# Kernel optimization log

Hardware: AMD Instinct MI355X
Metric: run time of the kernel (lower is better)

Reference implementation:

```python
import jax, jax.numpy as jnp
import numpy as np

NUM_HEADS = 16
MAX_BATCH = 4
MAX_SEQ = 2048


def setup_inputs() -> dict:
    key = jax.random.key(0)
    ks = jax.random.split(key, 9)
    B, S, H = 4, 2048, 2048
    scale = 0.02
    hidden_state = jax.random.normal(ks[0], (B, S, H), dtype=jnp.float32)
    # causal mask (masked_fill where mask == 0), broadcastable over batch/heads
    mask = jnp.tril(jnp.ones((S, S), dtype=jnp.int32))[None, None]  # [1,1,S,S]
    Wq = jax.random.normal(ks[1], (H, H), dtype=jnp.float32) * scale
    Wk = jax.random.normal(ks[2], (H, H), dtype=jnp.float32) * scale
    Wv = jax.random.normal(ks[3], (H, H), dtype=jnp.float32) * scale
    Wo = jax.random.normal(ks[4], (H, H), dtype=jnp.float32) * scale
    bq = jax.random.normal(ks[5], (H,), dtype=jnp.float32) * scale
    bk = jax.random.normal(ks[6], (H,), dtype=jnp.float32) * scale
    bv = jax.random.normal(ks[7], (H,), dtype=jnp.float32) * scale
    bo = jax.random.normal(ks[8], (H,), dtype=jnp.float32) * scale
    return {"hidden_state": hidden_state, "mask": mask,
            "Wq": Wq, "bq": bq, "Wk": Wk, "bk": bk,
            "Wv": Wv, "bv": bv, "Wo": Wo, "bo": bo,
            "start_pos": 0}


def reference(hidden_state, mask, Wq, bq, Wk, bk, Wv, bv, Wo, bo, start_pos):
    B, S, H = hidden_state.shape
    nh = NUM_HEADS
    hd = H // nh
    # qkv projections (nn.Linear: x @ W.T + b)
    q = (hidden_state @ Wq.T + bq).reshape(B, S, nh, hd)
    k = (hidden_state @ Wk.T + bk).reshape(B, S, nh, hd)
    v = (hidden_state @ Wv.T + bv).reshape(B, S, nh, hd)
    # KV-cache append (zeros-initialized buffer, write [start_pos:start_pos+S])
    cache_k = jnp.zeros((MAX_BATCH, MAX_SEQ, nh, hd), dtype=q.dtype)
    cache_v = jnp.zeros((MAX_BATCH, MAX_SEQ, nh, hd), dtype=q.dtype)
    cache_k = jax.lax.dynamic_update_slice(cache_k, k, (0, start_pos, 0, 0))
    cache_v = jax.lax.dynamic_update_slice(cache_v, v, (0, start_pos, 0, 0))
    total = start_pos + S
    key = cache_k[:B, :total]   # [B, total, nh, hd]
    value = cache_v[:B, :total]
    # scores: [B, nh, S, total]
    scores = jnp.einsum('bqhd,bkhd->bhqk', q, key) / jnp.sqrt(jnp.float32(hd))
    scores = jnp.where(mask == 0, -jnp.inf, scores)
    probs = jax.nn.softmax(scores, axis=-1)
    out = jnp.einsum('bhqk,bkhd->bqhd', probs, value).reshape(B, S, H)
    return out @ Wo.T + bo
```

## Files before the change

kernel.cpp:

```cpp
#include <hip/hip_runtime.h>
#include <hip/hip_bf16.h>
#include <stdint.h>

#define S_LEN 2048
#define HDIM  2048
#define NH    16
#define HD    128
#define BATCH 4

typedef __attribute__((ext_vector_type(8))) short bf16x8;
typedef __attribute__((ext_vector_type(4))) float f32x4;
typedef __attribute__((ext_vector_type(4))) float float4v;
typedef __attribute__((ext_vector_type(4))) unsigned short u16x4;

__device__ __forceinline__ void gload_lds16(const void* g, void* l) {
  __builtin_amdgcn_global_load_lds(
      (const __attribute__((address_space(1))) unsigned int*)g,
      (__attribute__((address_space(3))) unsigned int*)l,
      16, 0, 0);
}

__device__ __forceinline__ unsigned short f2bf(float x) {
  __hip_bfloat16 b = __float2bfloat16(x);
  return *reinterpret_cast<unsigned short*>(&b);
}

#define SL2E 0.1275174465f

__global__ __launch_bounds__(256) void cvt5_kernel(
    const float* __restrict__ x,
    const float* __restrict__ w0, const float* __restrict__ w1,
    const float* __restrict__ w2, const float* __restrict__ w3,
    unsigned short* __restrict__ ox,
    unsigned short* __restrict__ o0, unsigned short* __restrict__ o1,
    unsigned short* __restrict__ o2, unsigned short* __restrict__ o3,
    int n4x, int n4w) {
  const int y = blockIdx.y;
  const float* in = (y == 0) ? x : (y == 1) ? w0 : (y == 2) ? w1 : (y == 3) ? w2 : w3;
  unsigned short* out = (y == 0) ? ox : (y == 1) ? o0 : (y == 2) ? o1 : (y == 3) ? o2 : o3;
  const int n4 = (y == 0) ? n4x : n4w;
  int stride = gridDim.x * blockDim.x;
  for (int i = blockIdx.x * blockDim.x + threadIdx.x; i < n4; i += stride) {
    float4v v = *(const float4v*)(in + (size_t)i * 4);
    u16x4 o;
    o.x = f2bf(v.x); o.y = f2bf(v.y); o.z = f2bf(v.z); o.w = f2bf(v.w);
    *(u16x4*)(out + (size_t)i * 4) = o;
  }
}


#define G8_VMW(N) asm volatile("s_waitcnt vmcnt(" #N ")" ::: "memory")
#define G8_BAR1() do { __builtin_amdgcn_sched_barrier(0); __builtin_amdgcn_s_barrier(); \
  asm volatile("s_waitcnt lgkmcnt(0)" ::: "memory"); __builtin_amdgcn_sched_barrier(0); } while (0)
#define G8_BAR2() do { __builtin_amdgcn_sched_barrier(0); __builtin_amdgcn_s_barrier(); \
  __builtin_amdgcn_sched_barrier(0); } while (0)

#define G8_STAGE(ISB, BUF, HALF, KT) do {                                          \
  int kt_ = (KT); if (kt_ > nkt1) kt_ = nkt1;                                      \
  const char* gs_ = ((ISB) ? Bg : Ag) +                                            \
      (size_t)(((ISB) ? bn : bm) * 256 + (HALF) * 128 + w * 16) * (size_t)K2 +     \
      (size_t)kt_ * 128;                                                           \
  char* ld_ = lds + (BUF) * 65536 + (ISB) * 32768 + ((HALF) * 128 + w * 16) * 128; \
  gload_lds16(gs_ + sLn, ld_);                                                     \
  gload_lds16(gs_ + 8 * (size_t)K2 + sLn, ld_ + 1024);                             \
} while (0)

#define G8_RDA(BUF, MI0) do {                                                      \
  _Pragma("unroll") for (int mi = 0; mi < 4; ++mi)                                 \
  _Pragma("unroll") for (int kk = 0; kk < 2; ++kk)                                 \
    a[mi][kk] = *(const bf16x8*)(lds + (BUF) * 65536 +                             \
        (wm + ((MI0) + mi) * 16 + ln) * 128 + ((((kk << 2) + g) ^ ln7) << 4));     \
} while (0)

#define G8_RDB(BUF, NI0, BREG) do {                                                \
  _Pragma("unroll") for (int ni = 0; ni < 2; ++ni)                                 \
  _Pragma("unroll") for (int kk = 0; kk < 2; ++kk)                                 \
    BREG[ni][kk] = *(const bf16x8*)(lds + (BUF) * 65536 + 32768 +                  \
        (wn + ((NI0) + ni) * 16 + ln) * 128 + ((((kk << 2) + g) ^ ln7) << 4));     \
} while (0)

#define G8_MFMA(M0, N0, BREG) do {                                                 \
  __builtin_amdgcn_s_setprio(1);                                                   \
  _Pragma("unroll") for (int mi = 0; mi < 4; ++mi)                                 \
  _Pragma("unroll") for (int ni = 0; ni < 2; ++ni)                                 \
  _Pragma("unroll") for (int kk = 0; kk < 2; ++kk)                                 \
    acc[(M0) + mi][(N0) + ni] = __builtin_amdgcn_mfma_f32_16x16x32_bf16(           \
        a[mi][kk], BREG[ni][kk], acc[(M0) + mi][(N0) + ni], 0, 0, 0);              \
  __builtin_amdgcn_s_setprio(0);                                                   \
} while (0)

template<int OUTMODE>
__global__ __launch_bounds__(512, 2) void gemm8(
    const __hip_bfloat16* __restrict__ A, const __hip_bfloat16* __restrict__ B,
    const float* __restrict__ bias, void* __restrict__ C,
    int M, int N, int K, float scale) {
  __shared__ char lds[131072];
  const int tid = threadIdx.x;
  const int w = tid >> 6;
  const int lane = tid & 63;
  const int g = lane >> 4;
  const int ln = lane & 15;
  const int ln7 = lane & 7;
  const int K2 = K * 2;
  const int nkt = K >> 6;
  const int nkt1 = nkt - 1;
  const int niter = nkt >> 1;

  const int NBN = N >> 8;
  const int nwg = (M >> 8) * NBN;
  const int cpx = nwg >> 3;
  const int bid = blockIdx.x;
  const int wg = (bid & 7) * cpx + (bid >> 3);
  const int bm = wg / NBN, bn = wg % NBN;

  const int wm = (w >> 2) * 128;
  const int wn = (w & 3) * 64;

  const char* Ag = (const char*)A;
  const char* Bg = (const char*)B;
  const size_t sLn = (size_t)(lane >> 3) * (size_t)K2 +
                     (size_t)(((lane & 7) ^ (lane >> 3)) << 4);

  f32x4 acc[8][4];
#pragma unroll
  for (int mi = 0; mi < 8; ++mi)
#pragma unroll
    for (int ni = 0; ni < 4; ++ni) acc[mi][ni] = (f32x4){0.f, 0.f, 0.f, 0.f};

  G8_STAGE(0, 0, 0, 0); G8_STAGE(0, 0, 1, 0);
  G8_STAGE(1, 0, 0, 0); G8_STAGE(1, 0, 1, 0);
  G8_STAGE(1, 1, 0, 1); G8_STAGE(1, 1, 1, 1);
  G8_VMW(4);
  G8_BAR2();

  for (int i = 0; i < niter; ++i) {
    const int v = 2 * i + 1, u2 = 2 * i + 2, v2 = 2 * i + 3;
    bf16x8 a[4][2], b0[2][2], b1[2][2];
    G8_RDA(0, 0); G8_RDB(0, 0, b0);
    G8_STAGE(0, 1, 0, v);
    G8_BAR1();
    G8_MFMA(0, 0, b0);
    G8_BAR2();
    G8_RDB(0, 2, b1);
    G8_STAGE(0, 1, 1, v);
    G8_BAR1();
    G8_MFMA(0, 2, b1);
    G8_BAR2();
    G8_RDA(0, 4);
    G8_STAGE(1, 0, 0, u2);
    G8_BAR1();
    G8_MFMA(4, 0, b0);
    G8_BAR2();
    G8_STAGE(1, 0, 1, u2);
    G8_VMW(4);
    G8_BAR1();
    G8_MFMA(4, 2, b1);
    G8_BAR2();
    G8_RDA(1, 0); G8_RDB(1, 0, b0);
    G8_STAGE(0, 0, 0, u2);
    G8_BAR1();
    G8_MFMA(0, 0, b0);
    G8_BAR2();
    G8_RDB(1, 2, b1);
    G8_STAGE(0, 0, 1, u2);
    G8_BAR1();
    G8_MFMA(0, 2, b1);
    G8_BAR2();
    G8_RDA(1, 4);
    G8_STAGE(1, 1, 0, v2);
    G8_BAR1();
    G8_MFMA(4, 0, b0);
    G8_BAR2();
    G8_STAGE(1, 1, 1, v2);
    G8_VMW(4);
    G8_BAR1();
    G8_MFMA(4, 2, b1);
    G8_BAR2();
  }

  G8_VMW(0);
#pragma unroll
  for (int ni = 0; ni < 4; ++ni) {
    const int col = bn * 256 + wn + ni * 16 + ln;
    const float bv = bias[col];
#pragma unroll
    for (int mi = 0; mi < 8; ++mi) {
      const int row0 = bm * 256 + wm + mi * 16 + g * 4;
      if (OUTMODE == 2) {
        const int h = col >> 7, d = col & 127;
        const size_t base = ((size_t)((row0 >> 11) * NH + h) * HD + d) * S_LEN +
                            (row0 & (S_LEN - 1));
        u16x4 pk;
#pragma unroll
        for (int r = 0; r < 4; ++r)
          pk[r] = f2bf((acc[mi][ni][r] + bv) * scale);
        *(u16x4*)((unsigned short*)C + base) = pk;
      } else {
#pragma unroll
        for (int r = 0; r < 4; ++r) {
          float val = (acc[mi][ni][r] + bv) * scale;
          if (OUTMODE == 1)
            ((float*)C)[(size_t)(row0 + r) * N + col] = val;
          else
            ((__hip_bfloat16*)C)[(size_t)(row0 + r) * N + col] = __float2bfloat16(val);
        }
      }
    }
  }
}

#define DEFER_THR 8.0f

__global__ __launch_bounds__(256, 2) void attn_kernel(
    const __hip_bfloat16* __restrict__ Q, const __hip_bfloat16* __restrict__ Kg,
    const __hip_bfloat16* __restrict__ Vt, __hip_bfloat16* __restrict__ O) {
  __shared__ char lds[49152];
  const int tid = threadIdx.x;
  const int w = tid >> 6;
  const int lane = tid & 63;
  const int g = lane >> 4;
  const int ln = lane & 15;
  const int bh = blockIdx.x;
  const int pairid = blockIdx.y;
  const int b = bh >> 4, h = bh & 15;

  const char* Qb = (const char*)Q + ((size_t)b * S_LEN * HDIM + h * HD) * 2;
  const char* Kb = (const char*)Kg + ((size_t)b * S_LEN * HDIM + h * HD) * 2;
  const char* Vb = (const char*)Vt + ((size_t)bh * HD * S_LEN) * 2;
  char* ldsK = lds;
  char* ldsV = lds + 16384;
  char* pw   = lds + 32768 + w * 4096;

  const int kr = lane >> 4;
  const int kc = lane & 15;
  const int vr = lane >> 3;
  const int vc = lane & 7;

  auto stage = [&](int kv0) {
#pragma unroll
    for (int i = 0; i < 4; i++) {
      int r = w * 16 + i * 4 + kr;
      gload_lds16(Kb + (size_t)(kv0 + r) * (HDIM * 2) + ((kc ^ (r & 7)) << 4),
                  ldsK + (w * 16 + i * 4) * 256);
    }
#pragma unroll
    for (int i = 0; i < 4; i++) {
      int r = w * 32 + i * 8 + vr;
      gload_lds16(Vb + (size_t)r * (S_LEN * 2) + (size_t)kv0 * 2 + ((vc ^ vr) << 4),
                  ldsV + (w * 32 + i * 8) * 128);
    }
  };

  for (int pass = 0; pass < 2; pass++) {
    const int qt = pass == 0 ? (15 - pairid) : pairid;
    const int q0 = qt * 128 + w * 32;

    const int nt = 2 * qt + 2;
    __syncthreads();
    stage(0);

    bf16x8 qf[2][4];
#pragma unroll
    for (int qs = 0; qs < 2; qs++)
#pragma unroll
      for (int dc = 0; dc < 4; dc++)
        qf[qs][dc] = *(const bf16x8*)(Qb + (size_t)(q0 + qs * 16 + ln) * HDIM * 2 +
                                      (dc * 32 + g * 8) * 2);

    f32x4 o[2][8];
#pragma unroll
    for (int qs = 0; qs < 2; qs++)
#pragma unroll
      for (int ds = 0; ds < 8; ds++) o[qs][ds] = (f32x4){0.f, 0.f, 0.f, 0.f};
    float mrun[2][4], lrun[2][4];
#pragma unroll
    for (int qs = 0; qs < 2; qs++)
#pragma unroll
      for (int r = 0; r < 4; r++) { mrun[qs][r] = -__builtin_inff(); lrun[qs][r] = 0.f; }

    __syncthreads();

    for (int t = 0; t < nt; t++) {
      const int kv0 = t * 64;

      if (kv0 <= q0 + 31) {
        f32x4 sa[2][4];
#pragma unroll
        for (int qs = 0; qs < 2; qs++)
#pragma unroll
          for (int ks = 0; ks < 4; ks++) sa[qs][ks] = (f32x4){0.f, 0.f, 0.f, 0.f};
#pragma unroll
        for (int dc = 0; dc < 4; dc++) {
          bf16x8 kf[4];
#pragma unroll
          for (int ks = 0; ks < 4; ks++)
            kf[ks] = *(const bf16x8*)(ldsK + (ks * 16 + ln) * 256 +
                                      (((dc * 4 + g) ^ (ln & 7)) << 4));
          __builtin_amdgcn_s_setprio(1);
#pragma unroll
          for (int qs = 0; qs < 2; qs++)
#pragma unroll
            for (int ks = 0; ks < 4; ks++)
              sa[qs][ks] = __builtin_amdgcn_mfma_f32_16x16x32_bf16(qf[qs][dc], kf[ks], sa[qs][ks], 0, 0, 0);
          __builtin_amdgcn_s_setprio(0);
        }
        const bool needmask = (kv0 + 63) > q0;
        if (needmask) {
#pragma unroll
          for (int qs = 0; qs < 2; qs++)
#pragma unroll
            for (int ks = 0; ks < 4; ks++)
#pragma unroll
              for (int r = 0; r < 4; r++)
                if ((kv0 + ks * 16 + ln) > (q0 + qs * 16 + g * 4 + r))
                  sa[qs][ks][r] = -__builtin_inff();
        }
        float pmax[2][4];
#pragma unroll
        for (int qs = 0; qs < 2; qs++)
#pragma unroll
          for (int r = 0; r < 4; r++) {
            float mx = fmaxf(fmaxf(sa[qs][0][r], sa[qs][1][r]), fmaxf(sa[qs][2][r], sa[qs][3][r]));
            mx = fmaxf(mx, __shfl_xor(mx, 1));
            mx = fmaxf(mx, __shfl_xor(mx, 2));
            mx = fmaxf(mx, __shfl_xor(mx, 4));
            mx = fmaxf(mx, __shfl_xor(mx, 8));
            pmax[qs][r] = mx;
          }
        float dmin = 1e30f;
#pragma unroll
        for (int qs = 0; qs < 2; qs++)
#pragma unroll
          for (int r = 0; r < 4; r++)
            dmin = fminf(dmin, mrun[qs][r] + DEFER_THR - pmax[qs][r]);
        if (!__all(dmin >= 0.0f)) {
          float alpha[2][4];
#pragma unroll
          for (int qs = 0; qs < 2; qs++)
#pragma unroll
            for (int r = 0; r < 4; r++) {
              float mn = fmaxf(mrun[qs][r], pmax[qs][r]);
              alpha[qs][r] = exp2f(mrun[qs][r] - mn);
              mrun[qs][r] = mn;
              lrun[qs][r] *= alpha[qs][r];
            }
#pragma unroll
          for (int qs = 0; qs < 2; qs++)
#pragma unroll
            for (int ds = 0; ds < 8; ds++)
#pragma unroll
              for (int r = 0; r < 4; r++) o[qs][ds][r] *= alpha[qs][r];
        }
        float rsum[2][4];
#pragma unroll
        for (int qs = 0; qs < 2; qs++)
#pragma unroll
          for (int r = 0; r < 4; r++) rsum[qs][r] = 0.f;
#pragma unroll
        for (int qs = 0; qs < 2; qs++)
#pragma unroll
          for (int ks = 0; ks < 4; ks++)
#pragma unroll
            for (int r = 0; r < 4; r++) {
              float p = exp2f(sa[qs][ks][r] - mrun[qs][r]);
              sa[qs][ks][r] = p;
              rsum[qs][r] += p;
            }
#pragma unroll
        for (int qs = 0; qs < 2; qs++)
#pragma unroll
          for (int r = 0; r < 4; r++) {
            float rs = rsum[qs][r];
            rs += __shfl_xor(rs, 1);
            rs += __shfl_xor(rs, 2);
            rs += __shfl_xor(rs, 4);
            rs += __shfl_xor(rs, 8);
            lrun[qs][r] += rs;
          }
#pragma unroll
        for (int qs = 0; qs < 2; qs++)
#pragma unroll
          for (int ks = 0; ks < 4; ks++)
#pragma unroll
            for (int r = 0; r < 4; r++) {
              int row = qs * 16 + g * 4 + r;
              int key = ks * 16 + ln;
              *(__hip_bfloat16*)(pw + row * 128 + (((key >> 3) ^ (row & 7)) << 4) + (key & 7) * 2) =
                  __float2bfloat16(sa[qs][ks][r]);
            }
#pragma unroll
        for (int kk = 0; kk < 2; kk++) {
          bf16x8 pa[2];
#pragma unroll
          for (int qs = 0; qs < 2; qs++) {
            int row = qs * 16 + ln;
            pa[qs] = *(const bf16x8*)(pw + row * 128 + (((kk * 4 + g) ^ (row & 7)) << 4));
          }
          __builtin_amdgcn_s_setprio(1);
#pragma unroll
          for (int ds = 0; ds < 8; ds++) {
            bf16x8 vf = *(const bf16x8*)(ldsV + (ds * 16 + ln) * 128 +
                                         (((kk * 4 + g) ^ (ln & 7)) << 4));
#pragma unroll
            for (int qs = 0; qs < 2; qs++)
              o[qs][ds] = __builtin_amdgcn_mfma_f32_16x16x32_bf16(pa[qs], vf, o[qs][ds], 0, 0, 0);
          }
          __builtin_amdgcn_s_setprio(0);
        }
      }

      if (t + 1 < nt) {
        __syncthreads();
        stage(kv0 + 64);
        __syncthreads();
      }
    }
    float inv[2][4];
#pragma unroll
    for (int qs = 0; qs < 2; qs++)
#pragma unroll
      for (int r = 0; r < 4; r++) inv[qs][r] = 1.0f / lrun[qs][r];
    __hip_bfloat16* Ob = O + (size_t)b * S_LEN * HDIM + h * HD;
#pragma unroll
    for (int qs = 0; qs < 2; qs++)
#pragma unroll
      for (int ds = 0; ds < 8; ds++)
#pragma unroll
        for (int r = 0; r < 4; r++)
          Ob[(size_t)(q0 + qs * 16 + g * 4 + r) * HDIM + ds * 16 + ln] =
              __float2bfloat16(o[qs][ds][r] * inv[qs][r]);
  }
}

extern "C" void kernel_launch(void* const* d_in, const int* in_sizes, int n_in,
                              void* d_out, int out_size, void* d_ws, size_t ws_size,
                              hipStream_t stream) {
  const float* X  = (const float*)d_in[0];
  const float* Wq = (const float*)d_in[2];
  const float* bq = (const float*)d_in[3];
  const float* Wk = (const float*)d_in[4];
  const float* bk = (const float*)d_in[5];
  const float* Wv = (const float*)d_in[6];
  const float* bv = (const float*)d_in[7];
  const float* Wo = (const float*)d_in[8];
  const float* bo = (const float*)d_in[9];

  char* ws = (char*)d_ws;
  __hip_bfloat16* Xb   = (__hip_bfloat16*)(ws);
  __hip_bfloat16* Wqb  = (__hip_bfloat16*)(ws + 33554432);
  __hip_bfloat16* Wkb  = (__hip_bfloat16*)(ws + 41943040);
  __hip_bfloat16* Wvb  = (__hip_bfloat16*)(ws + 50331648);
  __hip_bfloat16* Wob  = (__hip_bfloat16*)(ws + 58720256);
  __hip_bfloat16* Qb   = (__hip_bfloat16*)(ws + 67108864);
  __hip_bfloat16* Kb   = (__hip_bfloat16*)(ws + 100663296);
  __hip_bfloat16* Ob   = (__hip_bfloat16*)(ws + 134217728);
  __hip_bfloat16* Vtb  = (__hip_bfloat16*)(ws + 167772160);

  cvt5_kernel<<<dim3(512, 5), 256, 0, stream>>>(
      X, Wq, Wk, Wv, Wo,
      (unsigned short*)Xb,
      (unsigned short*)Wqb, (unsigned short*)Wkb,
      (unsigned short*)Wvb, (unsigned short*)Wob,
      16777216 / 4, 4194304 / 4);

  gemm8<0><<<256, 512, 0, stream>>>(Xb, Wqb, bq, Qb,  8192, 2048, 2048, SL2E);
  gemm8<0><<<256, 512, 0, stream>>>(Xb, Wkb, bk, Kb,  8192, 2048, 2048, 1.0f);
  gemm8<2><<<256, 512, 0, stream>>>(Xb, Wvb, bv, Vtb, 8192, 2048, 2048, 1.0f);

  attn_kernel<<<dim3(64, 8), 256, 0, stream>>>(Qb, Kb, Vtb, Ob);

  gemm8<1><<<256, 512, 0, stream>>>(Ob, Wob, bo, (float*)d_out, 8192, 2048, 2048, 1.0f);
}
```

Before: 433.9 us.

## Shrink attention query tile to 64 rows with rebalanced causal work assignment

The attention kernel moves from 128-row query tiles (32 rows per wave) to 64-row tiles (16 rows per wave). The grid grows from 8 to 12 blocks per head, with a hand-built schedule that pairs long and short causal tiles so each block does a similar amount of work. LDS use and register pressure drop, which lets launch bounds request 3 blocks per SM. The cost is that each staged K/V tile is now shared by half as many query rows, so K/V traffic and barrier count per unit of work go up.

```diff
diff --git a/kernel.cpp b/kernel.cpp
--- a/kernel.cpp
+++ b/kernel.cpp
@@ -211,17 +211,17 @@
 
 #define DEFER_THR 8.0f
 
-__global__ __launch_bounds__(256, 2) void attn_kernel(
+__global__ __launch_bounds__(256, 3) void attn_kernel(
     const __hip_bfloat16* __restrict__ Q, const __hip_bfloat16* __restrict__ Kg,
     const __hip_bfloat16* __restrict__ Vt, __hip_bfloat16* __restrict__ O) {
-  __shared__ char lds[49152];
+  __shared__ char lds[40960];
   const int tid = threadIdx.x;
   const int w = tid >> 6;
   const int lane = tid & 63;
   const int g = lane >> 4;
   const int ln = lane & 15;
   const int bh = blockIdx.x;
-  const int pairid = blockIdx.y;
+  const int gy = blockIdx.y;
   const int b = bh >> 4, h = bh & 15;
 
   const char* Qb = (const char*)Q + ((size_t)b * S_LEN * HDIM + h * HD) * 2;
@@ -229,7 +229,7 @@
   const char* Vb = (const char*)Vt + ((size_t)bh * HD * S_LEN) * 2;
   char* ldsK = lds;
   char* ldsV = lds + 16384;
-  char* pw   = lds + 32768 + w * 4096;
+  char* pw   = lds + 32768 + w * 2048;
 
   const int kr = lane >> 4;
   const int kc = lane & 15;
@@ -251,44 +251,40 @@
     }
   };
 
-  for (int pass = 0; pass < 2; pass++) {
-    const int qt = pass == 0 ? (15 - pairid) : pairid;
-    const int q0 = qt * 128 + w * 32;
-
-    const int nt = 2 * qt + 2;
+  const int cnt = (gy < 10) ? 2 : (gy == 10) ? 4 : 8;
+  for (int pass = 0; pass < cnt; pass++) {
+    int qt;
+    if (gy < 10)       qt = (pass == 0) ? (31 - gy) : (11 + gy);
+    else if (gy == 10) qt = (pass == 0) ? 21 : (pass == 1) ? 10 : (pass == 2) ? 9 : 0;
+    else               qt = 8 - pass;
+    const int q0 = qt * 64 + w * 16;
+
+    const int nt = qt + 1;
     __syncthreads();
     stage(0);
 
-    bf16x8 qf[2][4];
-#pragma unroll
-    for (int qs = 0; qs < 2; qs++)
-#pragma unroll
-      for (int dc = 0; dc < 4; dc++)
-        qf[qs][dc] = *(const bf16x8*)(Qb + (size_t)(q0 + qs * 16 + ln) * HDIM * 2 +
-                                      (dc * 32 + g * 8) * 2);
-
-    f32x4 o[2][8];
-#pragma unroll
-    for (int qs = 0; qs < 2; qs++)
-#pragma unroll
-      for (int ds = 0; ds < 8; ds++) o[qs][ds] = (f32x4){0.f, 0.f, 0.f, 0.f};
-    float mrun[2][4], lrun[2][4];
-#pragma unroll
-    for (int qs = 0; qs < 2; qs++)
-#pragma unroll
-      for (int r = 0; r < 4; r++) { mrun[qs][r] = -__builtin_inff(); lrun[qs][r] = 0.f; }
+    bf16x8 qf[4];
+#pragma unroll
+    for (int dc = 0; dc < 4; dc++)
+      qf[dc] = *(const bf16x8*)(Qb + (size_t)(q0 + ln) * HDIM * 2 +
+                                (dc * 32 + g * 8) * 2);
+
+    f32x4 o[8];
+#pragma unroll
+    for (int ds = 0; ds < 8; ds++) o[ds] = (f32x4){0.f, 0.f, 0.f, 0.f};
+    float mrun[4], lrun[4];
+#pragma unroll
+    for (int r = 0; r < 4; r++) { mrun[r] = -__builtin_inff(); lrun[r] = 0.f; }
 
     __syncthreads();
 
     for (int t = 0; t < nt; t++) {
       const int kv0 = t * 64;
 
-      if (kv0 <= q0 + 31) {
-        f32x4 sa[2][4];
-#pragma unroll
-        for (int qs = 0; qs < 2; qs++)
-#pragma unroll
-          for (int ks = 0; ks < 4; ks++) sa[qs][ks] = (f32x4){0.f, 0.f, 0.f, 0.f};
+      if (kv0 <= q0 + 15) {
+        f32x4 sa[4];
+#pragma unroll
+        for (int ks = 0; ks < 4; ks++) sa[ks] = (f32x4){0.f, 0.f, 0.f, 0.f};
 #pragma unroll
         for (int dc = 0; dc < 4; dc++) {
           bf16x8 kf[4];
@@ -298,112 +294,85 @@
                                       (((dc * 4 + g) ^ (ln & 7)) << 4));
           __builtin_amdgcn_s_setprio(1);
 #pragma unroll
-          for (int qs = 0; qs < 2; qs++)
-#pragma unroll
-            for (int ks = 0; ks < 4; ks++)
-              sa[qs][ks] = __builtin_amdgcn_mfma_f32_16x16x32_bf16(qf[qs][dc], kf[ks], sa[qs][ks], 0, 0, 0);
+          for (int ks = 0; ks < 4; ks++)
+            sa[ks] = __builtin_amdgcn_mfma_f32_16x16x32_bf16(qf[dc], kf[ks], sa[ks], 0, 0, 0);
           __builtin_amdgcn_s_setprio(0);
         }
         const bool needmask = (kv0 + 63) > q0;
         if (needmask) {
 #pragma unroll
-          for (int qs = 0; qs < 2; qs++)
-#pragma unroll
-            for (int ks = 0; ks < 4; ks++)
-#pragma unroll
-              for (int r = 0; r < 4; r++)
-                if ((kv0 + ks * 16 + ln) > (q0 + qs * 16 + g * 4 + r))
-                  sa[qs][ks][r] = -__builtin_inff();
-        }
-        float pmax[2][4];
-#pragma unroll
-        for (int qs = 0; qs < 2; qs++)
+          for (int ks = 0; ks < 4; ks++)
+#pragma unroll
+            for (int r = 0; r < 4; r++)
+              if ((kv0 + ks * 16 + ln) > (q0 + g * 4 + r))
+                sa[ks][r] = -__builtin_inff();
+        }
+        float pmax[4];
+#pragma unroll
+        for (int r = 0; r < 4; r++) {
+          float mx = fmaxf(fmaxf(sa[0][r], sa[1][r]), fmaxf(sa[2][r], sa[3][r]));
+          mx = fmaxf(mx, __shfl_xor(mx, 1));
+          mx = fmaxf(mx, __shfl_xor(mx, 2));
+          mx = fmaxf(mx, __shfl_xor(mx, 4));
+          mx = fmaxf(mx, __shfl_xor(mx, 8));
+          pmax[r] = mx;
+        }
+        float dmin = 1e30f;
+#pragma unroll
+        for (int r = 0; r < 4; r++)
+          dmin = fminf(dmin, mrun[r] + DEFER_THR - pmax[r]);
+        if (!__all(dmin >= 0.0f)) {
+          float alpha[4];
 #pragma unroll
           for (int r = 0; r < 4; r++) {
-            float mx = fmaxf(fmaxf(sa[qs][0][r], sa[qs][1][r]), fmaxf(sa[qs][2][r], sa[qs][3][r]));
-            mx = fmaxf(mx, __shfl_xor(mx, 1));
-            mx = fmaxf(mx, __shfl_xor(mx, 2));
-            mx = fmaxf(mx, __shfl_xor(mx, 4));
-            mx = fmaxf(mx, __shfl_xor(mx, 8));
-            pmax[qs][r] = mx;
+            float mn = fmaxf(mrun[r], pmax[r]);
+            alpha[r] = exp2f(mrun[r] - mn);
+            mrun[r] = mn;
+            lrun[r] *= alpha[r];
           }
-        float dmin = 1e30f;
-#pragma unroll
-        for (int qs = 0; qs < 2; qs++)
-#pragma unroll
-          for (int r = 0; r < 4; r++)
-            dmin = fminf(dmin, mrun[qs][r] + DEFER_THR - pmax[qs][r]);
-        if (!__all(dmin >= 0.0f)) {
-          float alpha[2][4];
-#pragma unroll
-          for (int qs = 0; qs < 2; qs++)
-#pragma unroll
-            for (int r = 0; r < 4; r++) {
-              float mn = fmaxf(mrun[qs][r], pmax[qs][r]);
-              alpha[qs][r] = exp2f(mrun[qs][r] - mn);
-              mrun[qs][r] = mn;
-              lrun[qs][r] *= alpha[qs][r];
-            }
-#pragma unroll
-          for (int qs = 0; qs < 2; qs++)
-#pragma unroll
-            for (int ds = 0; ds < 8; ds++)
-#pragma unroll
-              for (int r = 0; r < 4; r++) o[qs][ds][r] *= alpha[qs][r];
-        }
-        float rsum[2][4];
-#pragma unroll
-        for (int qs = 0; qs < 2; qs++)
-#pragma unroll
-          for (int r = 0; r < 4; r++) rsum[qs][r] = 0.f;
-#pragma unroll
-        for (int qs = 0; qs < 2; qs++)
-#pragma unroll
-          for (int ks = 0; ks < 4; ks++)
-#pragma unroll
-            for (int r = 0; r < 4; r++) {
-              float p = exp2f(sa[qs][ks][r] - mrun[qs][r]);
-              sa[qs][ks][r] = p;
-              rsum[qs][r] += p;
-            }
-#pragma unroll
-        for (int qs = 0; qs < 2; qs++)
+#pragma unroll
+          for (int ds = 0; ds < 8; ds++)
+#pragma unroll
+            for (int r = 0; r < 4; r++) o[ds][r] *= alpha[r];
+        }
+        float rsum[4];
+#pragma unroll
+        for (int r = 0; r < 4; r++) rsum[r] = 0.f;
+#pragma unroll
+        for (int ks = 0; ks < 4; ks++)
 #pragma unroll
           for (int r = 0; r < 4; r++) {
-            float rs = rsum[qs][r];
-            rs += __shfl_xor(rs, 1);
-            rs += __shfl_xor(rs, 2);
-            rs += __shfl_xor(rs, 4);
-            rs += __shfl_xor(rs, 8);
-            lrun[qs][r] += rs;
+            float p = exp2f(sa[ks][r] - mrun[r]);
+            sa[ks][r] = p;
+            rsum[r] += p;
           }
 #pragma unroll
-        for (int qs = 0; qs < 2; qs++)
-#pragma unroll
-          for (int ks = 0; ks < 4; ks++)
-#pragma unroll
-            for (int r = 0; r < 4; r++) {
-              int row = qs * 16 + g * 4 + r;
-              int key = ks * 16 + ln;
-              *(__hip_bfloat16*)(pw + row * 128 + (((key >> 3) ^ (row & 7)) << 4) + (key & 7) * 2) =
-                  __float2bfloat16(sa[qs][ks][r]);
-            }
+        for (int r = 0; r < 4; r++) {
+          float rs = rsum[r];
+          rs += __shfl_xor(rs, 1);
+          rs += __shfl_xor(rs, 2);
+          rs += __shfl_xor(rs, 4);
+          rs += __shfl_xor(rs, 8);
+          lrun[r] += rs;
+        }
+#pragma unroll
+        for (int ks = 0; ks < 4; ks++)
+#pragma unroll
+          for (int r = 0; r < 4; r++) {
+            int row = g * 4 + r;
+            int key = ks * 16 + ln;
+            *(__hip_bfloat16*)(pw + row * 128 + (((key >> 3) ^ (row & 7)) << 4) + (key & 7) * 2) =
+                __float2bfloat16(sa[ks][r]);
+          }
 #pragma unroll
         for (int kk = 0; kk < 2; kk++) {
-          bf16x8 pa[2];
-#pragma unroll
-          for (int qs = 0; qs < 2; qs++) {
-            int row = qs * 16 + ln;
-            pa[qs] = *(const bf16x8*)(pw + row * 128 + (((kk * 4 + g) ^ (row & 7)) << 4));
-          }
+          bf16x8 pa = *(const bf16x8*)(pw + ln * 128 + (((kk * 4 + g) ^ (ln & 7)) << 4));
           __builtin_amdgcn_s_setprio(1);
 #pragma unroll
           for (int ds = 0; ds < 8; ds++) {
             bf16x8 vf = *(const bf16x8*)(ldsV + (ds * 16 + ln) * 128 +
                                          (((kk * 4 + g) ^ (ln & 7)) << 4));
-#pragma unroll
-            for (int qs = 0; qs < 2; qs++)
-              o[qs][ds] = __builtin_amdgcn_mfma_f32_16x16x32_bf16(pa[qs], vf, o[qs][ds], 0, 0, 0);
+            o[ds] = __builtin_amdgcn_mfma_f32_16x16x32_bf16(pa, vf, o[ds], 0, 0, 0);
           }
           __builtin_amdgcn_s_setprio(0);
         }
@@ -415,20 +384,16 @@
         __syncthreads();
       }
     }
-    float inv[2][4];
-#pragma unroll
-    for (int qs = 0; qs < 2; qs++)
-#pragma unroll
-      for (int r = 0; r < 4; r++) inv[qs][r] = 1.0f / lrun[qs][r];
+    float inv[4];
+#pragma unroll
+    for (int r = 0; r < 4; r++) inv[r] = 1.0f / lrun[r];
     __hip_bfloat16* Ob = O + (size_t)b * S_LEN * HDIM + h * HD;
 #pragma unroll
-    for (int qs = 0; qs < 2; qs++)
-#pragma unroll
-      for (int ds = 0; ds < 8; ds++)
-#pragma unroll
-        for (int r = 0; r < 4; r++)
-          Ob[(size_t)(q0 + qs * 16 + g * 4 + r) * HDIM + ds * 16 + ln] =
-              __float2bfloat16(o[qs][ds][r] * inv[qs][r]);
+    for (int ds = 0; ds < 8; ds++)
+#pragma unroll
+      for (int r = 0; r < 4; r++)
+        Ob[(size_t)(q0 + g * 4 + r) * HDIM + ds * 16 + ln] =
+            __float2bfloat16(o[ds][r] * inv[r]);
   }
 }
 
@@ -467,7 +432,7 @@
   gemm8<0><<<256, 512, 0, stream>>>(Xb, Wkb, bk, Kb,  8192, 2048, 2048, 1.0f);
   gemm8<2><<<256, 512, 0, stream>>>(Xb, Wvb, bv, Vtb, 8192, 2048, 2048, 1.0f);
 
-  attn_kernel<<<dim3(64, 8), 256, 0, stream>>>(Qb, Kb, Vtb, Ob);
+  attn_kernel<<<dim3(64, 12), 256, 0, stream>>>(Qb, Kb, Vtb, Ob);
 
   gemm8<1><<<256, 512, 0, stream>>>(Ob, Wob, bo, (float*)d_out, 8192, 2048, 2048, 1.0f);
 }
```

After: 453.0 us. +4.4%, slower.
